# Optimization experiments

Measured on AMD Instinct MI355X. Metric: run time of the kernel, lower is better.

The kernel has to match this reference:

```python
import jax, jax.numpy as jnp
import numpy as np
from jax import lax

T, D, I, E = 4096, 1024, 1024, 32
TOP_K = 4
ROUTED_SCALING = 1.0
EPS = 1e-6


def setup_inputs() -> dict:
    key = jax.random.key(0)
    k1, k2, k3, k4, k5 = jax.random.split(key, 5)
    return {
        "hidden_states": jax.random.normal(k1, (T, D), dtype=jnp.float32),
        "gate_w": jax.random.normal(k2, (E, D), dtype=jnp.float32) * 0.02,
        "gate_up_proj": jax.random.normal(k3, (E, 2 * I, D), dtype=jnp.float32) * 0.02,
        "down_proj": jax.random.normal(k4, (E, D, I), dtype=jnp.float32) * 0.02,
        "expert_bias": jax.random.normal(k5, (E,), dtype=jnp.float32) * 0.01,
    }


def _route(hidden_states, gate_w, expert_bias):
    # router_logits: [T, E]
    logits = hidden_states @ gate_w.T
    routing_weights = jax.nn.sigmoid(logits)
    # expert bias affects selection only, not the weights
    scores = routing_weights + expert_bias[None, :]
    _, selected = lax.top_k(scores, TOP_K)                      # [T, K] int32
    w = jnp.take_along_axis(routing_weights, selected, axis=1)  # [T, K]
    w = w / (w.sum(axis=-1, keepdims=True) + EPS)               # norm_topk_prob
    w = w * ROUTED_SCALING
    return selected, w


def reference(hidden_states, gate_w, gate_up_proj, down_proj, expert_bias):
    t, d = hidden_states.shape
    selected, w = _route(hidden_states, gate_w, expert_bias)
    # dense token->expert combine weights [T, E] (top_k indices are unique per row)
    comb = jnp.zeros((t, E), dtype=hidden_states.dtype)
    comb = comb.at[jnp.arange(t)[:, None], selected].add(w)

    def body(acc, xs):
        w_gu, w_d, cw = xs                       # [2I,D], [D,I], [T]
        gu = hidden_states @ w_gu.T              # [T, 2I]
        g, u = jnp.split(gu, 2, axis=-1)
        h = jax.nn.silu(g) * u                   # [T, I]
        out = h @ w_d.T                          # [T, D]
        return acc + out * cw[:, None], None

    init = jnp.zeros_like(hidden_states)
    final, _ = lax.scan(body, init, (gate_up_proj, down_proj, comb.T))
    return final
```

## Files before the change

### kernel.cpp

```cpp
#include <hip/hip_runtime.h>
#include <hip/hip_bf16.h>
#include <cstdint>
#include <cstddef>

#define T_TOK 4096
#define DIM   1024
#define IDIM  1024
#define NEXP  32
#define TOPK  4
#define MAXT  160
#define RPAD  (MAXT*128)

typedef short sh8   __attribute__((ext_vector_type(8)));
typedef float f32x4 __attribute__((ext_vector_type(4)));

__device__ __forceinline__ short bf(float f) {
    union { float f; uint32_t u; } v; v.f = f;
    uint32_t r = (v.u + 0x7FFFu + ((v.u >> 16) & 1u)) >> 16;
    return (short)r;
}
__device__ __forceinline__ sh8 pack8(float4 a, float4 b) {
    sh8 r;
    r[0]=bf(a.x); r[1]=bf(a.y); r[2]=bf(a.z); r[3]=bf(a.w);
    r[4]=bf(b.x); r[5]=bf(b.y); r[6]=bf(b.z); r[7]=bf(b.w);
    return r;
}
__device__ __forceinline__ uint32_t cvtpk(float lo, float hi) {
    uint32_t r;
    asm("v_cvt_pk_bf16_f32 %0, %1, %2" : "=v"(r) : "v"(lo), "v"(hi));
    return r;
}
__device__ __forceinline__ sh8 cvt8(f32x4 a, f32x4 b) {
    union { uint32_t u[4]; sh8 s; } v;
    v.u[0] = cvtpk(a[0], a[1]); v.u[1] = cvtpk(a[2], a[3]);
    v.u[2] = cvtpk(b[0], b[1]); v.u[3] = cvtpk(b[2], b[3]);
    return v.s;
}
__device__ __forceinline__ void glds16(const void* g, const void* l) {
    __builtin_amdgcn_global_load_lds((const __attribute__((address_space(1))) void*)g,
                                     (__attribute__((address_space(3))) void*)l, 16, 0, 0);
}

__device__ __forceinline__ int tile_expert(const int* __restrict__ cnt, int mt, int& tile_start) {
    int s = 0, e = -1, ts = 0;
    #pragma unroll
    for (int i = 0; i < NEXP; ++i) {
        int t = (cnt[i] + 127) >> 7;
        if (mt >= s && mt < s + t) { e = i; ts = s; }
        s += t;
    }
    tile_start = ts;
    return e;
}

__device__ __forceinline__ int balanced_bid(const int* __restrict__ cnt, int ntsz) {
    int tb = 0;
    #pragma unroll
    for (int i = 0; i < NEXP; ++i) tb += (cnt[i] + 127) >> 7;
    int total = tb * ntsz;
    int q = total >> 3, r = total & 7;
    int xcd = (int)blockIdx.x & 7, pos = (int)blockIdx.x >> 3;
    int cap = q + (xcd < r ? 1 : 0);
    if (pos >= cap) return -1;
    return (xcd < r ? xcd * (q + 1) : r * (q + 1) + (xcd - r) * q) + pos;
}

__device__ __forceinline__ bool decode_wmajor(const int* __restrict__ cnt, int bid, int ntsz,
                                              int& e, int& mt, int& nt) {
    int base = 0, tacc = 0, fe = -1, floc = 0, fts = 0, fntl = 1;
    #pragma unroll
    for (int i = 0; i < NEXP; ++i) {
        int ntl = (cnt[i] + 127) >> 7;
        int sz  = ntsz * ntl;
        if (bid >= base && bid < base + sz) { fe = i; floc = bid - base; fts = tacc; fntl = ntl; }
        base += sz; tacc += ntl;
    }
    if (fe < 0) return false;
    e  = fe;
    nt = floc / fntl;
    mt = fts + (floc % fntl);
    return true;
}

__global__ __launch_bounds__(256) void router_kernel(
    const float* __restrict__ X, const float* __restrict__ GW,
    const float* __restrict__ bias, int* __restrict__ topk_idx,
    float* __restrict__ topk_w, int* __restrict__ cnt,
    int* __restrict__ tlist_c, int* __restrict__ posmap)
{
    int wid  = threadIdx.x >> 6;
    int lane = threadIdx.x & 63;
    int t = blockIdx.x * 4 + wid;

    float4 h[4];
    const float4* xr = reinterpret_cast<const float4*>(X + (size_t)t * DIM);
    #pragma unroll
    for (int c = 0; c < 4; ++c) h[c] = xr[lane + 64 * c];

    float myscore = 0.f;
    for (int e = 0; e < NEXP; ++e) {
        const float4* gr = reinterpret_cast<const float4*>(GW + (size_t)e * DIM);
        float p = 0.f;
        #pragma unroll
        for (int c = 0; c < 4; ++c) {
            float4 g = gr[lane + 64 * c];
            p += h[c].x * g.x + h[c].y * g.y + h[c].z * g.z + h[c].w * g.w;
        }
        #pragma unroll
        for (int o = 32; o; o >>= 1) p += __shfl_xor(p, o);
        if (lane == e) myscore = p;
    }
    float rw = 1.f / (1.f + expf(-myscore));
    float sel = (lane < NEXP) ? rw + bias[lane] : -1e30f;

    float wsum = 0.f;
    int   oi = 0; float ow = 0.f;
    #pragma unroll
    for (int k = 0; k < TOPK; ++k) {
        float v = sel;
        int   idx = (lane < NEXP) ? lane : 9999;
        #pragma unroll
        for (int o = 32; o; o >>= 1) {
            float v2 = __shfl_xor(v, o);
            int   i2 = __shfl_xor(idx, o);
            if (v2 > v || (v2 == v && i2 < idx)) { v = v2; idx = i2; }
        }
        float wk = __shfl(rw, idx);
        wsum += wk;
        if (lane == k)   { oi = idx; ow = wk; }
        if (lane == idx) sel = -1e30f;
    }
    if (lane < TOPK) {
        int gid = t * TOPK + lane;
        topk_idx[gid] = oi;
        topk_w  [gid] = ow / (wsum + 1e-6f);
        int pos = atomicAdd(&cnt[oi], 1);
        tlist_c[oi * T_TOK + pos] = t;
        posmap[gid] = pos;
    }
}

__global__ __launch_bounds__(256) void gather_kernel(
    const float* __restrict__ X, const int* __restrict__ cnt,
    const int* __restrict__ tlist_c, short* __restrict__ Xg)
{
    int wid = threadIdx.x >> 6, lane = threadIdx.x & 63;
    int r = blockIdx.x * 4 + wid;
    int ts;
    int e = tile_expert(cnt, r >> 7, ts);
    if (e < 0) return;
    int li = r - (ts << 7);
    bool real = li < cnt[e];
    int t = real ? tlist_c[e * T_TOK + li] : 0;
    const float4* src = reinterpret_cast<const float4*>(X + (size_t)t * DIM);
    sh8* dst = reinterpret_cast<sh8*>(Xg + (size_t)r * DIM);
    float4 z = make_float4(0.f, 0.f, 0.f, 0.f);
    #pragma unroll
    for (int it = 0; it < 2; ++it) {
        int si = it * 64 + lane;
        float4 a = real ? src[2 * si]     : z;
        float4 b = real ? src[2 * si + 1] : z;
        dst[si] = pack8(a, b);
    }
}

__global__ __launch_bounds__(256, 3) void gemm1_kernel(
    const short* __restrict__ Xg, const float* __restrict__ GUP,
    const int* __restrict__ cnt, short* __restrict__ H)
{
    int bid = balanced_bid(cnt, 16);
    if (bid < 0) return;
    int e, mt, nt;
    if (!decode_wmajor(cnt, bid, 16, e, mt, nt)) return;
    int m0 = mt * 128, n0 = nt * 64;

    __shared__ short As[128 * 64];
    __shared__ float Bg[64 * 64];
    __shared__ float Bu[64 * 64];

    int tid = threadIdx.x, lane = tid & 63, wv = tid >> 6;
    int wm = (wv >> 1) * 64, wn = (wv & 1) * 32;

    f32x4 accg[4][2] = {};
    f32x4 accu[4][2] = {};

    int swcolA = ((lane & 7) ^ (lane >> 3)) * 8;
    const float* gbase = GUP + ((size_t)e * 2 * IDIM + n0) * DIM;
    const float* ubase = gbase + (size_t)IDIM * DIM;

    auto stage = [&](int k0) {
        #pragma unroll
        for (int j = 0; j < 4; ++j) {
            int ch = wv * 4 + j;
            glds16(Xg + (size_t)(m0 + ch * 8 + (lane >> 3)) * DIM + k0 + swcolA, &As[ch * 512]);
        }
        #pragma unroll
        for (int j = 0; j < 4; ++j) {
            int ch = wv * 4 + j;
            int r  = ch * 4 + (lane >> 4);
            int sc = ((lane & 15) ^ (r & 15)) << 2;
            glds16(gbase + (size_t)r * DIM + k0 + sc, &Bg[ch * 256]);
            glds16(ubase + (size_t)r * DIM + k0 + sc, &Bu[ch * 256]);
        }
    };

    int swrA = (lane & 7) << 3;
    int rx   = lane & 15;
    for (int it = 0; it < DIM / 64; ++it) {
        stage(it * 64);
        __syncthreads();
        #pragma unroll
        for (int kk = 0; kk < 64; kk += 32) {
            int kiA = (kk + (lane >> 4) * 8) ^ swrA;
            sh8 af[4], gf[2], uf[2];
            #pragma unroll
            for (int fm = 0; fm < 4; ++fm)
                af[fm] = *reinterpret_cast<const sh8*>(&As[(wm + fm * 16 + (lane & 15)) * 64 + kiA]);
            int c0 = (kk >> 2) + (lane >> 4) * 2;
            #pragma unroll
            for (int fn = 0; fn < 2; ++fn) {
                int R = wn + fn * 16 + (lane & 15);
                const float* bg = &Bg[R * 64];
                f32x4 lo = *reinterpret_cast<const f32x4*>(&bg[(c0       ^ rx) << 2]);
                f32x4 hi = *reinterpret_cast<const f32x4*>(&bg[((c0 + 1) ^ rx) << 2]);
                gf[fn] = cvt8(lo, hi);
                const float* bu = &Bu[R * 64];
                lo = *reinterpret_cast<const f32x4*>(&bu[(c0       ^ rx) << 2]);
                hi = *reinterpret_cast<const f32x4*>(&bu[((c0 + 1) ^ rx) << 2]);
                uf[fn] = cvt8(lo, hi);
            }
            #pragma unroll
            for (int fm = 0; fm < 4; ++fm)
                #pragma unroll
                for (int fn = 0; fn < 2; ++fn) {
                    accg[fm][fn] = __builtin_amdgcn_mfma_f32_16x16x32_bf16(af[fm], gf[fn], accg[fm][fn], 0, 0, 0);
                    accu[fm][fn] = __builtin_amdgcn_mfma_f32_16x16x32_bf16(af[fm], uf[fn], accu[fm][fn], 0, 0, 0);
                }
        }
        __syncthreads();
    }

    #pragma unroll
    for (int fm = 0; fm < 4; ++fm)
        #pragma unroll
        for (int r = 0; r < 4; ++r) {
            int row = m0 + wm + fm * 16 + (lane >> 4) * 4 + r;
            #pragma unroll
            for (int fn = 0; fn < 2; ++fn) {
                int col = n0 + wn + fn * 16 + (lane & 15);
                float g = accg[fm][fn][r];
                float u = accu[fm][fn][r];
                H[(size_t)row * IDIM + col] = bf(g / (1.f + expf(-g)) * u);
            }
        }
}

__global__ __launch_bounds__(256, 3) void gemm2_kernel(
    const short* __restrict__ H, const float* __restrict__ DP,
    const int* __restrict__ cnt, float* __restrict__ Yf)
{
    int bid = balanced_bid(cnt, 8);
    if (bid < 0) return;
    int e, mt, nt;
    if (!decode_wmajor(cnt, bid, 8, e, mt, nt)) return;
    int m0 = mt * 128, n0 = nt * 128;

    __shared__ short As[128 * 64];
    __shared__ float Bs[128 * 64];

    int tid = threadIdx.x, lane = tid & 63, wv = tid >> 6;
    int wm = (wv >> 1) * 64, wn = (wv & 1) * 64;

    f32x4 acc[4][4] = {};

    int swcolA = ((lane & 7) ^ (lane >> 3)) * 8;
    const float* dbase = DP + ((size_t)e * DIM + n0) * IDIM;

    auto stage = [&](int k0) {
        #pragma unroll
        for (int j = 0; j < 4; ++j) {
            int ch = wv * 4 + j;
            glds16(H + (size_t)(m0 + ch * 8 + (lane >> 3)) * IDIM + k0 + swcolA, &As[ch * 512]);
        }
        #pragma unroll
        for (int j = 0; j < 8; ++j) {
            int ch = wv * 8 + j;
            int r  = ch * 4 + (lane >> 4);
            int sc = ((lane & 15) ^ (r & 15)) << 2;
            glds16(dbase + (size_t)r * IDIM + k0 + sc, &Bs[ch * 256]);
        }
    };

    int swrA = (lane & 7) << 3;
    int rx   = lane & 15;
    for (int it = 0; it < IDIM / 64; ++it) {
        stage(it * 64);
        __syncthreads();
        #pragma unroll
        for (int kk = 0; kk < 64; kk += 32) {
            int kiA = (kk + (lane >> 4) * 8) ^ swrA;
            sh8 af[4], bq[4];
            #pragma unroll
            for (int fm = 0; fm < 4; ++fm)
                af[fm] = *reinterpret_cast<const sh8*>(&As[(wm + fm * 16 + (lane & 15)) * 64 + kiA]);
            int c0 = (kk >> 2) + (lane >> 4) * 2;
            #pragma unroll
            for (int fn = 0; fn < 4; ++fn) {
                int R = wn + fn * 16 + (lane & 15);
                const float* bs = &Bs[R * 64];
                f32x4 lo = *reinterpret_cast<const f32x4*>(&bs[(c0       ^ rx) << 2]);
                f32x4 hi = *reinterpret_cast<const f32x4*>(&bs[((c0 + 1) ^ rx) << 2]);
                bq[fn] = cvt8(lo, hi);
            }
            #pragma unroll
            for (int fm = 0; fm < 4; ++fm)
                #pragma unroll
                for (int fn = 0; fn < 4; ++fn)
                    acc[fm][fn] = __builtin_amdgcn_mfma_f32_16x16x32_bf16(af[fm], bq[fn], acc[fm][fn], 0, 0, 0);
        }
        __syncthreads();
    }

    #pragma unroll
    for (int fm = 0; fm < 4; ++fm)
        #pragma unroll
        for (int r = 0; r < 4; ++r) {
            int row = m0 + wm + fm * 16 + (lane >> 4) * 4 + r;
            #pragma unroll
            for (int fn = 0; fn < 4; ++fn) {
                int col = n0 + wn + fn * 16 + (lane & 15);
                Yf[(size_t)row * DIM + col] = acc[fm][fn][r];
            }
        }
}

__global__ __launch_bounds__(256) void combine_kernel(
    const float* __restrict__ Yf, const int* __restrict__ cnt,
    const int* __restrict__ topk_idx, const float* __restrict__ topk_w,
    const int* __restrict__ posmap, float* __restrict__ out)
{
    int t = blockIdx.x;
    int d = threadIdx.x * 4;
    int es[TOPK], rows[TOPK];
    #pragma unroll
    for (int k = 0; k < TOPK; ++k) es[k] = topk_idx[t * TOPK + k];
    int p = 0;
    #pragma unroll
    for (int i = 0; i < NEXP; ++i) {
        #pragma unroll
        for (int k = 0; k < TOPK; ++k)
            if (es[k] == i) rows[k] = p + posmap[t * TOPK + k];
        p += ((cnt[i] + 127) >> 7) << 7;
    }
    float4 acc = make_float4(0.f, 0.f, 0.f, 0.f);
    #pragma unroll
    for (int k = 0; k < TOPK; ++k) {
        float w = topk_w[t * TOPK + k];
        float4 y = *reinterpret_cast<const float4*>(Yf + (size_t)rows[k] * DIM + d);
        acc.x += w * y.x; acc.y += w * y.y; acc.z += w * y.z; acc.w += w * y.w;
    }
    *reinterpret_cast<float4*>(out + (size_t)t * DIM + d) = acc;
}

extern "C" void kernel_launch(void* const* d_in, const int* in_sizes, int n_in,
                              void* d_out, int out_size, void* d_ws, size_t ws_size,
                              hipStream_t stream)
{
    const float* X    = (const float*)d_in[0];
    const float* GW   = (const float*)d_in[1];
    const float* GUP  = (const float*)d_in[2];
    const float* DP   = (const float*)d_in[3];
    const float* BIAS = (const float*)d_in[4];
    float* out = (float*)d_out;

    char* ws = (char*)d_ws;
    int*   cnt      = (int*)ws;
    int*   topk_idx = (int*)(ws + (4u   << 10));
    float* topk_w   = (float*)(ws + (68u  << 10));
    int*   posmap   = (int*)(ws + (132u << 10));
    int*   tlist_c  = (int*)(ws + (196u << 10));

    constexpr size_t OFF_H  = 2ull << 20;
    constexpr size_t SZ_BF  = (size_t)RPAD * IDIM * 2;
    constexpr size_t OFF_XG = OFF_H + SZ_BF;
    constexpr size_t OFF_YF = OFF_XG + SZ_BF;

    short* H  = (short*)(ws + OFF_H);
    short* Xg = (short*)(ws + OFF_XG);
    float* Yf = (float*)(ws + OFF_YF);

    (void)hipMemsetAsync(cnt, 0, 128, stream);

    router_kernel<<<T_TOK / 4, 256, 0, stream>>>(X, GW, BIAS, topk_idx, topk_w,
                                                 cnt, tlist_c, posmap);
    gather_kernel<<<RPAD / 4, 256, 0, stream>>>(X, cnt, tlist_c, Xg);

    gemm1_kernel<<<MAXT * 16, 256, 0, stream>>>(Xg, GUP, cnt, H);
    gemm2_kernel<<<MAXT * 8,  256, 0, stream>>>(H, DP, cnt, Yf);

    combine_kernel<<<T_TOK, 256, 0, stream>>>(Yf, cnt, topk_idx, topk_w, posmap, out);
}
```

Measured before the change: 329.0 us.

## Double-buffer LDS staging in both expert GEMMs with K-step of 32

Both grouped GEMM kernels now split the shared-memory tiles into two buffers of half the K depth (32 instead of 64). The next tile's global-to-LDS loads are issued before computing on the current one, and a partial vmcnt wait replaces the full synchronisation. This aims to hide global memory latency behind MFMA work. Total LDS use stays the same, but there are twice as many iterations and barriers, and correctness now depends on the hand-counted vmcnt(6) matching the number of outstanding loads.

```diff
diff --git a/kernel.cpp b/kernel.cpp
--- a/kernel.cpp
+++ b/kernel.cpp
@@ -174,9 +174,9 @@
     if (!decode_wmajor(cnt, bid, 16, e, mt, nt)) return;
     int m0 = mt * 128, n0 = nt * 64;
 
-    __shared__ short As[128 * 64];
-    __shared__ float Bg[64 * 64];
-    __shared__ float Bu[64 * 64];
+    __shared__ short As[2][128 * 32];
+    __shared__ float Bg[2][64 * 32];
+    __shared__ float Bu[2][64 * 32];
 
     int tid = threadIdx.x, lane = tid & 63, wv = tid >> 6;
     int wm = (wv >> 1) * 64, wn = (wv & 1) * 32;
@@ -184,60 +184,71 @@
     f32x4 accg[4][2] = {};
     f32x4 accu[4][2] = {};
 
-    int swcolA = ((lane & 7) ^ (lane >> 3)) * 8;
+    const short* abase = Xg + (size_t)m0 * DIM;
     const float* gbase = GUP + ((size_t)e * 2 * IDIM + n0) * DIM;
     const float* ubase = gbase + (size_t)IDIM * DIM;
 
-    auto stage = [&](int k0) {
-        #pragma unroll
-        for (int j = 0; j < 4; ++j) {
-            int ch = wv * 4 + j;
-            glds16(Xg + (size_t)(m0 + ch * 8 + (lane >> 3)) * DIM + k0 + swcolA, &As[ch * 512]);
-        }
-        #pragma unroll
-        for (int j = 0; j < 4; ++j) {
-            int ch = wv * 4 + j;
-            int r  = ch * 4 + (lane >> 4);
-            int sc = ((lane & 15) ^ (r & 15)) << 2;
-            glds16(gbase + (size_t)r * DIM + k0 + sc, &Bg[ch * 256]);
-            glds16(ubase + (size_t)r * DIM + k0 + sc, &Bu[ch * 256]);
+    int aRow = lane >> 2;
+    int aCol = ((lane & 3) ^ (aRow & 3)) * 8;
+    int bRow = lane >> 3;
+    int bCol = ((lane & 7) ^ bRow) * 4;
+
+    auto stage = [&](int b, int k0) {
+        #pragma unroll
+        for (int j = 0; j < 2; ++j) {
+            int ch = wv * 2 + j;
+            glds16(abase + (size_t)(ch * 16 + aRow) * DIM + k0 + aCol, &As[b][ch * 512]);
+        }
+        #pragma unroll
+        for (int j = 0; j < 2; ++j) {
+            int ch = wv * 2 + j;
+            glds16(gbase + (size_t)(ch * 8 + bRow) * DIM + k0 + bCol, &Bg[b][ch * 256]);
+            glds16(ubase + (size_t)(ch * 8 + bRow) * DIM + k0 + bCol, &Bu[b][ch * 256]);
         }
     };
 
-    int swrA = (lane & 7) << 3;
-    int rx   = lane & 15;
-    for (int it = 0; it < DIM / 64; ++it) {
-        stage(it * 64);
-        __syncthreads();
-        #pragma unroll
-        for (int kk = 0; kk < 64; kk += 32) {
-            int kiA = (kk + (lane >> 4) * 8) ^ swrA;
-            sh8 af[4], gf[2], uf[2];
-            #pragma unroll
-            for (int fm = 0; fm < 4; ++fm)
-                af[fm] = *reinterpret_cast<const sh8*>(&As[(wm + fm * 16 + (lane & 15)) * 64 + kiA]);
-            int c0 = (kk >> 2) + (lane >> 4) * 2;
+    int aIdx = ((lane >> 4) ^ (lane & 3)) * 8;
+    int c0b  = (lane >> 4) * 2;
+    int rxB  = lane & 7;
+
+    stage(0, 0);
+    for (int it = 0; it < DIM / 32; ++it) {
+        int c = it & 1;
+        if (it + 1 < DIM / 32) {
+            stage(c ^ 1, (it + 1) * 32);
+            asm volatile("s_waitcnt vmcnt(6)" ::: "memory");
+        } else {
+            asm volatile("s_waitcnt vmcnt(0)" ::: "memory");
+        }
+        __builtin_amdgcn_sched_barrier(0);
+        __builtin_amdgcn_s_barrier();
+
+        sh8 af[4], gf[2], uf[2];
+        #pragma unroll
+        for (int fm = 0; fm < 4; ++fm)
+            af[fm] = *reinterpret_cast<const sh8*>(&As[c][(wm + fm * 16 + (lane & 15)) * 32 + aIdx]);
+        #pragma unroll
+        for (int fn = 0; fn < 2; ++fn) {
+            int R = wn + fn * 16 + (lane & 15);
+            const float* bg = &Bg[c][R * 32];
+            f32x4 lo = *reinterpret_cast<const f32x4*>(&bg[( c0b      ^ rxB) << 2]);
+            f32x4 hi = *reinterpret_cast<const f32x4*>(&bg[((c0b + 1) ^ rxB) << 2]);
+            gf[fn] = cvt8(lo, hi);
+            const float* bu = &Bu[c][R * 32];
+            lo = *reinterpret_cast<const f32x4*>(&bu[( c0b      ^ rxB) << 2]);
+            hi = *reinterpret_cast<const f32x4*>(&bu[((c0b + 1) ^ rxB) << 2]);
+            uf[fn] = cvt8(lo, hi);
+        }
+        #pragma unroll
+        for (int fm = 0; fm < 4; ++fm)
             #pragma unroll
             for (int fn = 0; fn < 2; ++fn) {
-                int R = wn + fn * 16 + (lane & 15);
-                const float* bg = &Bg[R * 64];
-                f32x4 lo = *reinterpret_cast<const f32x4*>(&bg[(c0       ^ rx) << 2]);
-                f32x4 hi = *reinterpret_cast<const f32x4*>(&bg[((c0 + 1) ^ rx) << 2]);
-                gf[fn] = cvt8(lo, hi);
-                const float* bu = &Bu[R * 64];
-                lo = *reinterpret_cast<const f32x4*>(&bu[(c0       ^ rx) << 2]);
-                hi = *reinterpret_cast<const f32x4*>(&bu[((c0 + 1) ^ rx) << 2]);
-                uf[fn] = cvt8(lo, hi);
+                accg[fm][fn] = __builtin_amdgcn_mfma_f32_16x16x32_bf16(af[fm], gf[fn], accg[fm][fn], 0, 0, 0);
+                accu[fm][fn] = __builtin_amdgcn_mfma_f32_16x16x32_bf16(af[fm], uf[fn], accu[fm][fn], 0, 0, 0);
             }
-            #pragma unroll
-            for (int fm = 0; fm < 4; ++fm)
-                #pragma unroll
-                for (int fn = 0; fn < 2; ++fn) {
-                    accg[fm][fn] = __builtin_amdgcn_mfma_f32_16x16x32_bf16(af[fm], gf[fn], accg[fm][fn], 0, 0, 0);
-                    accu[fm][fn] = __builtin_amdgcn_mfma_f32_16x16x32_bf16(af[fm], uf[fn], accu[fm][fn], 0, 0, 0);
-                }
-        }
-        __syncthreads();
+
+        asm volatile("" ::: "memory");
+        __builtin_amdgcn_s_barrier();
     }
 
     #pragma unroll
@@ -265,60 +276,71 @@
     if (!decode_wmajor(cnt, bid, 8, e, mt, nt)) return;
     int m0 = mt * 128, n0 = nt * 128;
 
-    __shared__ short As[128 * 64];
-    __shared__ float Bs[128 * 64];
+    __shared__ short As[2][128 * 32];
+    __shared__ float Bs[2][128 * 32];
 
     int tid = threadIdx.x, lane = tid & 63, wv = tid >> 6;
     int wm = (wv >> 1) * 64, wn = (wv & 1) * 64;
 
     f32x4 acc[4][4] = {};
 
-    int swcolA = ((lane & 7) ^ (lane >> 3)) * 8;
+    const short* abase = H + (size_t)m0 * IDIM;
     const float* dbase = DP + ((size_t)e * DIM + n0) * IDIM;
 
-    auto stage = [&](int k0) {
+    int aRow = lane >> 2;
+    int aCol = ((lane & 3) ^ (aRow & 3)) * 8;
+    int bRow = lane >> 3;
+    int bCol = ((lane & 7) ^ bRow) * 4;
+
+    auto stage = [&](int b, int k0) {
+        #pragma unroll
+        for (int j = 0; j < 2; ++j) {
+            int ch = wv * 2 + j;
+            glds16(abase + (size_t)(ch * 16 + aRow) * IDIM + k0 + aCol, &As[b][ch * 512]);
+        }
         #pragma unroll
         for (int j = 0; j < 4; ++j) {
             int ch = wv * 4 + j;
-            glds16(H + (size_t)(m0 + ch * 8 + (lane >> 3)) * IDIM + k0 + swcolA, &As[ch * 512]);
-        }
-        #pragma unroll
-        for (int j = 0; j < 8; ++j) {
-            int ch = wv * 8 + j;
-            int r  = ch * 4 + (lane >> 4);
-            int sc = ((lane & 15) ^ (r & 15)) << 2;
-            glds16(dbase + (size_t)r * IDIM + k0 + sc, &Bs[ch * 256]);
+            glds16(dbase + (size_t)(ch * 8 + bRow) * IDIM + k0 + bCol, &Bs[b][ch * 256]);
         }
     };
 
-    int swrA = (lane & 7) << 3;
-    int rx   = lane & 15;
-    for (int it = 0; it < IDIM / 64; ++it) {
-        stage(it * 64);
-        __syncthreads();
-        #pragma unroll
-        for (int kk = 0; kk < 64; kk += 32) {
-            int kiA = (kk + (lane >> 4) * 8) ^ swrA;
-            sh8 af[4], bq[4];
+    int aIdx = ((lane >> 4) ^ (lane & 3)) * 8;
+    int c0b  = (lane >> 4) * 2;
+    int rxB  = lane & 7;
+
+    stage(0, 0);
+    for (int it = 0; it < IDIM / 32; ++it) {
+        int c = it & 1;
+        if (it + 1 < IDIM / 32) {
+            stage(c ^ 1, (it + 1) * 32);
+            asm volatile("s_waitcnt vmcnt(6)" ::: "memory");
+        } else {
+            asm volatile("s_waitcnt vmcnt(0)" ::: "memory");
+        }
+        __builtin_amdgcn_sched_barrier(0);
+        __builtin_amdgcn_s_barrier();
+
+        sh8 af[4], bq[4];
+        #pragma unroll
+        for (int fm = 0; fm < 4; ++fm)
+            af[fm] = *reinterpret_cast<const sh8*>(&As[c][(wm + fm * 16 + (lane & 15)) * 32 + aIdx]);
+        #pragma unroll
+        for (int fn = 0; fn < 4; ++fn) {
+            int R = wn + fn * 16 + (lane & 15);
+            const float* bs = &Bs[c][R * 32];
+            f32x4 lo = *reinterpret_cast<const f32x4*>(&bs[( c0b      ^ rxB) << 2]);
+            f32x4 hi = *reinterpret_cast<const f32x4*>(&bs[((c0b + 1) ^ rxB) << 2]);
+            bq[fn] = cvt8(lo, hi);
+        }
+        #pragma unroll
+        for (int fm = 0; fm < 4; ++fm)
             #pragma unroll
-            for (int fm = 0; fm < 4; ++fm)
-                af[fm] = *reinterpret_cast<const sh8*>(&As[(wm + fm * 16 + (lane & 15)) * 64 + kiA]);
-            int c0 = (kk >> 2) + (lane >> 4) * 2;
-            #pragma unroll
-            for (int fn = 0; fn < 4; ++fn) {
-                int R = wn + fn * 16 + (lane & 15);
-                const float* bs = &Bs[R * 64];
-                f32x4 lo = *reinterpret_cast<const f32x4*>(&bs[(c0       ^ rx) << 2]);
-                f32x4 hi = *reinterpret_cast<const f32x4*>(&bs[((c0 + 1) ^ rx) << 2]);
-                bq[fn] = cvt8(lo, hi);
-            }
-            #pragma unroll
-            for (int fm = 0; fm < 4; ++fm)
-                #pragma unroll
-                for (int fn = 0; fn < 4; ++fn)
-                    acc[fm][fn] = __builtin_amdgcn_mfma_f32_16x16x32_bf16(af[fm], bq[fn], acc[fm][fn], 0, 0, 0);
-        }
-        __syncthreads();
+            for (int fn = 0; fn < 4; ++fn)
+                acc[fm][fn] = __builtin_amdgcn_mfma_f32_16x16x32_bf16(af[fm], bq[fn], acc[fm][fn], 0, 0, 0);
+
+        asm volatile("" ::: "memory");
+        __builtin_amdgcn_s_barrier();
     }
 
     #pragma unroll
```

After: 370.3 us. 1.13x slower.

## Load fp32 expert weights straight to registers and double-buffer activation tiles

Applied to the files above, without the earlier changes.

Both expert GEMMs now read their fp32 weight fragments directly from global memory into registers, prefetched one k-step ahead, instead of staging them through LDS. The activation tile is double-buffered in LDS, so each iteration needs one barrier instead of two. gemm2 also drops to a 64-wide N tile with twice the blocks and raises its occupancy hint to 4. The intent is to cut LDS traffic and barrier stalls and to overlap loads with MFMA work. In exchange, weight loads become less coalesced (strided per-lane rows) and each block reuses the streamed weights less.

```diff
diff --git a/kernel.cpp b/kernel.cpp
--- a/kernel.cpp
+++ b/kernel.cpp
@@ -174,61 +174,65 @@
     if (!decode_wmajor(cnt, bid, 16, e, mt, nt)) return;
     int m0 = mt * 128, n0 = nt * 64;
 
-    __shared__ short As[128 * 64];
-    __shared__ float Bg[64 * 64];
-    __shared__ float Bu[64 * 64];
+    __shared__ short As[2][128 * 64];
 
     int tid = threadIdx.x, lane = tid & 63, wv = tid >> 6;
     int wm = (wv >> 1) * 64, wn = (wv & 1) * 32;
+    int l15 = lane & 15;
 
     f32x4 accg[4][2] = {};
     f32x4 accu[4][2] = {};
 
     int swcolA = ((lane & 7) ^ (lane >> 3)) * 8;
-    const float* gbase = GUP + ((size_t)e * 2 * IDIM + n0) * DIM;
-    const float* ubase = gbase + (size_t)IDIM * DIM;
-
-    auto stage = [&](int k0) {
+    int swrA   = (lane & 7) << 3;
+
+    const float* gp[2];
+    const float* up[2];
+    #pragma unroll
+    for (int fn = 0; fn < 2; ++fn) {
+        gp[fn] = GUP + ((size_t)e * 2 * IDIM + n0 + wn + fn * 16 + l15) * DIM + (lane >> 4) * 8;
+        up[fn] = gp[fn] + (size_t)IDIM * DIM;
+    }
+
+    f32x4 bg[4], bu[4];
+    auto loadB = [&](int k) {
+        #pragma unroll
+        for (int fn = 0; fn < 2; ++fn) {
+            bg[fn * 2]     = *reinterpret_cast<const f32x4*>(gp[fn] + k);
+            bg[fn * 2 + 1] = *reinterpret_cast<const f32x4*>(gp[fn] + k + 4);
+            bu[fn * 2]     = *reinterpret_cast<const f32x4*>(up[fn] + k);
+            bu[fn * 2 + 1] = *reinterpret_cast<const f32x4*>(up[fn] + k + 4);
+        }
+    };
+    auto stageA = [&](int b, int k0) {
         #pragma unroll
         for (int j = 0; j < 4; ++j) {
             int ch = wv * 4 + j;
-            glds16(Xg + (size_t)(m0 + ch * 8 + (lane >> 3)) * DIM + k0 + swcolA, &As[ch * 512]);
-        }
-        #pragma unroll
-        for (int j = 0; j < 4; ++j) {
-            int ch = wv * 4 + j;
-            int r  = ch * 4 + (lane >> 4);
-            int sc = ((lane & 15) ^ (r & 15)) << 2;
-            glds16(gbase + (size_t)r * DIM + k0 + sc, &Bg[ch * 256]);
-            glds16(ubase + (size_t)r * DIM + k0 + sc, &Bu[ch * 256]);
+            glds16(Xg + (size_t)(m0 + ch * 8 + (lane >> 3)) * DIM + k0 + swcolA, &As[b][ch * 512]);
         }
     };
 
-    int swrA = (lane & 7) << 3;
-    int rx   = lane & 15;
+    loadB(0);
+    stageA(0, 0);
     for (int it = 0; it < DIM / 64; ++it) {
-        stage(it * 64);
+        int b = it & 1;
         __syncthreads();
-        #pragma unroll
-        for (int kk = 0; kk < 64; kk += 32) {
-            int kiA = (kk + (lane >> 4) * 8) ^ swrA;
-            sh8 af[4], gf[2], uf[2];
+        if (it + 1 < DIM / 64) stageA(b ^ 1, (it + 1) * 64);
+        #pragma unroll
+        for (int kh = 0; kh < 2; ++kh) {
+            sh8 gf[2], uf[2];
+            #pragma unroll
+            for (int fn = 0; fn < 2; ++fn) {
+                gf[fn] = cvt8(bg[fn * 2], bg[fn * 2 + 1]);
+                uf[fn] = cvt8(bu[fn * 2], bu[fn * 2 + 1]);
+            }
+            int nk = it * 64 + (kh + 1) * 32;
+            if (nk < DIM) loadB(nk);
+            int kiA = (kh * 32 + (lane >> 4) * 8) ^ swrA;
+            sh8 af[4];
             #pragma unroll
             for (int fm = 0; fm < 4; ++fm)
-                af[fm] = *reinterpret_cast<const sh8*>(&As[(wm + fm * 16 + (lane & 15)) * 64 + kiA]);
-            int c0 = (kk >> 2) + (lane >> 4) * 2;
-            #pragma unroll
-            for (int fn = 0; fn < 2; ++fn) {
-                int R = wn + fn * 16 + (lane & 15);
-                const float* bg = &Bg[R * 64];
-                f32x4 lo = *reinterpret_cast<const f32x4*>(&bg[(c0       ^ rx) << 2]);
-                f32x4 hi = *reinterpret_cast<const f32x4*>(&bg[((c0 + 1) ^ rx) << 2]);
-                gf[fn] = cvt8(lo, hi);
-                const float* bu = &Bu[R * 64];
-                lo = *reinterpret_cast<const f32x4*>(&bu[(c0       ^ rx) << 2]);
-                hi = *reinterpret_cast<const f32x4*>(&bu[((c0 + 1) ^ rx) << 2]);
-                uf[fn] = cvt8(lo, hi);
-            }
+                af[fm] = *reinterpret_cast<const sh8*>(&As[b][(wm + fm * 16 + l15) * 64 + kiA]);
             #pragma unroll
             for (int fm = 0; fm < 4; ++fm)
                 #pragma unroll
@@ -237,7 +241,6 @@
                     accu[fm][fn] = __builtin_amdgcn_mfma_f32_16x16x32_bf16(af[fm], uf[fn], accu[fm][fn], 0, 0, 0);
                 }
         }
-        __syncthreads();
     }
 
     #pragma unroll
@@ -247,7 +250,7 @@
             int row = m0 + wm + fm * 16 + (lane >> 4) * 4 + r;
             #pragma unroll
             for (int fn = 0; fn < 2; ++fn) {
-                int col = n0 + wn + fn * 16 + (lane & 15);
+                int col = n0 + wn + fn * 16 + l15;
                 float g = accg[fm][fn][r];
                 float u = accu[fm][fn][r];
                 H[(size_t)row * IDIM + col] = bf(g / (1.f + expf(-g)) * u);
@@ -255,70 +258,73 @@
         }
 }
 
-__global__ __launch_bounds__(256, 3) void gemm2_kernel(
+__global__ __launch_bounds__(256, 4) void gemm2_kernel(
     const short* __restrict__ H, const float* __restrict__ DP,
     const int* __restrict__ cnt, float* __restrict__ Yf)
 {
-    int bid = balanced_bid(cnt, 8);
+    int bid = balanced_bid(cnt, 16);
     if (bid < 0) return;
     int e, mt, nt;
-    if (!decode_wmajor(cnt, bid, 8, e, mt, nt)) return;
-    int m0 = mt * 128, n0 = nt * 128;
-
-    __shared__ short As[128 * 64];
-    __shared__ float Bs[128 * 64];
+    if (!decode_wmajor(cnt, bid, 16, e, mt, nt)) return;
+    int m0 = mt * 128, n0 = nt * 64;
+
+    __shared__ short As[2][128 * 64];
 
     int tid = threadIdx.x, lane = tid & 63, wv = tid >> 6;
-    int wm = (wv >> 1) * 64, wn = (wv & 1) * 64;
-
-    f32x4 acc[4][4] = {};
+    int wm = (wv >> 1) * 64, wn = (wv & 1) * 32;
+    int l15 = lane & 15;
+
+    f32x4 acc[4][2] = {};
 
     int swcolA = ((lane & 7) ^ (lane >> 3)) * 8;
-    const float* dbase = DP + ((size_t)e * DIM + n0) * IDIM;
-
-    auto stage = [&](int k0) {
+    int swrA   = (lane & 7) << 3;
+
+    const float* dp[2];
+    #pragma unroll
+    for (int fn = 0; fn < 2; ++fn)
+        dp[fn] = DP + ((size_t)e * DIM + n0 + wn + fn * 16 + l15) * IDIM + (lane >> 4) * 8;
+
+    f32x4 bd[4];
+    auto loadB = [&](int k) {
+        #pragma unroll
+        for (int fn = 0; fn < 2; ++fn) {
+            bd[fn * 2]     = *reinterpret_cast<const f32x4*>(dp[fn] + k);
+            bd[fn * 2 + 1] = *reinterpret_cast<const f32x4*>(dp[fn] + k + 4);
+        }
+    };
+    auto stageA = [&](int b, int k0) {
         #pragma unroll
         for (int j = 0; j < 4; ++j) {
             int ch = wv * 4 + j;
-            glds16(H + (size_t)(m0 + ch * 8 + (lane >> 3)) * IDIM + k0 + swcolA, &As[ch * 512]);
-        }
-        #pragma unroll
-        for (int j = 0; j < 8; ++j) {
-            int ch = wv * 8 + j;
-            int r  = ch * 4 + (lane >> 4);
-            int sc = ((lane & 15) ^ (r & 15)) << 2;
-            glds16(dbase + (size_t)r * IDIM + k0 + sc, &Bs[ch * 256]);
+            glds16(H + (size_t)(m0 + ch * 8 + (lane >> 3)) * IDIM + k0 + swcolA, &As[b][ch * 512]);
         }
     };
 
-    int swrA = (lane & 7) << 3;
-    int rx   = lane & 15;
+    loadB(0);
+    stageA(0, 0);
     for (int it = 0; it < IDIM / 64; ++it) {
-        stage(it * 64);
+        int b = it & 1;
         __syncthreads();
-        #pragma unroll
-        for (int kk = 0; kk < 64; kk += 32) {
-            int kiA = (kk + (lane >> 4) * 8) ^ swrA;
-            sh8 af[4], bq[4];
+        if (it + 1 < IDIM / 64) stageA(b ^ 1, (it + 1) * 64);
+        #pragma unroll
+        for (int kh = 0; kh < 2; ++kh) {
+            sh8 bq[2];
+            #pragma unroll
+            for (int fn = 0; fn < 2; ++fn)
+                bq[fn] = cvt8(bd[fn * 2], bd[fn * 2 + 1]);
+            int nk = it * 64 + (kh + 1) * 32;
+            if (nk < IDIM) loadB(nk);
+            int kiA = (kh * 32 + (lane >> 4) * 8) ^ swrA;
+            sh8 af[4];
             #pragma unroll
             for (int fm = 0; fm < 4; ++fm)
-                af[fm] = *reinterpret_cast<const sh8*>(&As[(wm + fm * 16 + (lane & 15)) * 64 + kiA]);
-            int c0 = (kk >> 2) + (lane >> 4) * 2;
-            #pragma unroll
-            for (int fn = 0; fn < 4; ++fn) {
-                int R = wn + fn * 16 + (lane & 15);
-                const float* bs = &Bs[R * 64];
-                f32x4 lo = *reinterpret_cast<const f32x4*>(&bs[(c0       ^ rx) << 2]);
-                f32x4 hi = *reinterpret_cast<const f32x4*>(&bs[((c0 + 1) ^ rx) << 2]);
-                bq[fn] = cvt8(lo, hi);
-            }
+                af[fm] = *reinterpret_cast<const sh8*>(&As[b][(wm + fm * 16 + l15) * 64 + kiA]);
             #pragma unroll
             for (int fm = 0; fm < 4; ++fm)
                 #pragma unroll
-                for (int fn = 0; fn < 4; ++fn)
+                for (int fn = 0; fn < 2; ++fn)
                     acc[fm][fn] = __builtin_amdgcn_mfma_f32_16x16x32_bf16(af[fm], bq[fn], acc[fm][fn], 0, 0, 0);
         }
-        __syncthreads();
     }
 
     #pragma unroll
@@ -327,8 +333,8 @@
         for (int r = 0; r < 4; ++r) {
             int row = m0 + wm + fm * 16 + (lane >> 4) * 4 + r;
             #pragma unroll
-            for (int fn = 0; fn < 4; ++fn) {
-                int col = n0 + wn + fn * 16 + (lane & 15);
+            for (int fn = 0; fn < 2; ++fn) {
+                int col = n0 + wn + fn * 16 + l15;
                 Yf[(size_t)row * DIM + col] = acc[fm][fn][r];
             }
         }
@@ -396,7 +402,7 @@
     gather_kernel<<<RPAD / 4, 256, 0, stream>>>(X, cnt, tlist_c, Xg);
 
     gemm1_kernel<<<MAXT * 16, 256, 0, stream>>>(Xg, GUP, cnt, H);
-    gemm2_kernel<<<MAXT * 8,  256, 0, stream>>>(H, DP, cnt, Yf);
+    gemm2_kernel<<<MAXT * 16, 256, 0, stream>>>(H, DP, cnt, Yf);
 
     combine_kernel<<<T_TOK, 256, 0, stream>>>(Yf, cnt, topk_idx, topk_w, posmap, out);
 }
```

Measured after the change: 603.9 us (median of 2 runs). +83.6%, slower.

## Pre-convert down_proj to bf16 inside gemm1 grid and load bf16 in gemm2

Applied to the files above, without the earlier changes.

Appends extra blocks to the gemm1 launch that convert the fp32 down_proj weights to bf16 in a workspace buffer. gemm2 then stages bf16 B tiles with the same swizzled layout as A, which halves its shared memory for B and drops the per-iteration fp32-to-bf16 conversion. The cost is a full conversion pass over all 32 experts' down weights (128MB read, 64MB written) every call, including experts with few tokens. That pass shares the gemm1 launch and may overlap with or delay its blocks.

```diff
diff --git a/kernel.cpp b/kernel.cpp
--- a/kernel.cpp
+++ b/kernel.cpp
@@ -10,6 +10,8 @@
 #define TOPK  4
 #define MAXT  160
 #define RPAD  (MAXT*128)
+#define G1_BLOCKS (MAXT*16)
+#define CONV_BLOCKS 8192
 
 typedef short sh8   __attribute__((ext_vector_type(8)));
 typedef float f32x4 __attribute__((ext_vector_type(4)));
@@ -166,8 +168,19 @@
 
 __global__ __launch_bounds__(256, 3) void gemm1_kernel(
     const short* __restrict__ Xg, const float* __restrict__ GUP,
+    const float* __restrict__ DP, short* __restrict__ Wdb,
     const int* __restrict__ cnt, short* __restrict__ H)
 {
+    if (blockIdx.x >= G1_BLOCKS) {
+        size_t i = ((size_t)(blockIdx.x - G1_BLOCKS) * 256 + threadIdx.x) * 16;
+        f32x4 a = *reinterpret_cast<const f32x4*>(DP + i);
+        f32x4 b = *reinterpret_cast<const f32x4*>(DP + i + 4);
+        f32x4 c = *reinterpret_cast<const f32x4*>(DP + i + 8);
+        f32x4 d = *reinterpret_cast<const f32x4*>(DP + i + 12);
+        *reinterpret_cast<sh8*>(Wdb + i)     = cvt8(a, b);
+        *reinterpret_cast<sh8*>(Wdb + i + 8) = cvt8(c, d);
+        return;
+    }
     int bid = balanced_bid(cnt, 16);
     if (bid < 0) return;
     int e, mt, nt;
@@ -256,7 +269,7 @@
 }
 
 __global__ __launch_bounds__(256, 3) void gemm2_kernel(
-    const short* __restrict__ H, const float* __restrict__ DP,
+    const short* __restrict__ H, const short* __restrict__ Wdb,
     const int* __restrict__ cnt, float* __restrict__ Yf)
 {
     int bid = balanced_bid(cnt, 8);
@@ -266,15 +279,16 @@
     int m0 = mt * 128, n0 = nt * 128;
 
     __shared__ short As[128 * 64];
-    __shared__ float Bs[128 * 64];
+    __shared__ short Bs[128 * 64];
 
     int tid = threadIdx.x, lane = tid & 63, wv = tid >> 6;
     int wm = (wv >> 1) * 64, wn = (wv & 1) * 64;
+    int l15 = lane & 15;
 
     f32x4 acc[4][4] = {};
 
     int swcolA = ((lane & 7) ^ (lane >> 3)) * 8;
-    const float* dbase = DP + ((size_t)e * DIM + n0) * IDIM;
+    const short* bbase = Wdb + ((size_t)e * DIM + n0) * IDIM;
 
     auto stage = [&](int k0) {
         #pragma unroll
@@ -283,35 +297,26 @@
             glds16(H + (size_t)(m0 + ch * 8 + (lane >> 3)) * IDIM + k0 + swcolA, &As[ch * 512]);
         }
         #pragma unroll
-        for (int j = 0; j < 8; ++j) {
-            int ch = wv * 8 + j;
-            int r  = ch * 4 + (lane >> 4);
-            int sc = ((lane & 15) ^ (r & 15)) << 2;
-            glds16(dbase + (size_t)r * IDIM + k0 + sc, &Bs[ch * 256]);
+        for (int j = 0; j < 4; ++j) {
+            int ch = wv * 4 + j;
+            glds16(bbase + (size_t)(ch * 8 + (lane >> 3)) * IDIM + k0 + swcolA, &Bs[ch * 512]);
         }
     };
 
-    int swrA = (lane & 7) << 3;
-    int rx   = lane & 15;
+    int swr = (lane & 7) << 3;
     for (int it = 0; it < IDIM / 64; ++it) {
         stage(it * 64);
         __syncthreads();
         #pragma unroll
         for (int kk = 0; kk < 64; kk += 32) {
-            int kiA = (kk + (lane >> 4) * 8) ^ swrA;
+            int ki = (kk + (lane >> 4) * 8) ^ swr;
             sh8 af[4], bq[4];
             #pragma unroll
             for (int fm = 0; fm < 4; ++fm)
-                af[fm] = *reinterpret_cast<const sh8*>(&As[(wm + fm * 16 + (lane & 15)) * 64 + kiA]);
-            int c0 = (kk >> 2) + (lane >> 4) * 2;
-            #pragma unroll
-            for (int fn = 0; fn < 4; ++fn) {
-                int R = wn + fn * 16 + (lane & 15);
-                const float* bs = &Bs[R * 64];
-                f32x4 lo = *reinterpret_cast<const f32x4*>(&bs[(c0       ^ rx) << 2]);
-                f32x4 hi = *reinterpret_cast<const f32x4*>(&bs[((c0 + 1) ^ rx) << 2]);
-                bq[fn] = cvt8(lo, hi);
-            }
+                af[fm] = *reinterpret_cast<const sh8*>(&As[(wm + fm * 16 + l15) * 64 + ki]);
+            #pragma unroll
+            for (int fn = 0; fn < 4; ++fn)
+                bq[fn] = *reinterpret_cast<const sh8*>(&Bs[(wn + fn * 16 + l15) * 64 + ki]);
             #pragma unroll
             for (int fm = 0; fm < 4; ++fm)
                 #pragma unroll
@@ -328,7 +333,7 @@
             int row = m0 + wm + fm * 16 + (lane >> 4) * 4 + r;
             #pragma unroll
             for (int fn = 0; fn < 4; ++fn) {
-                int col = n0 + wn + fn * 16 + (lane & 15);
+                int col = n0 + wn + fn * 16 + l15;
                 Yf[(size_t)row * DIM + col] = acc[fm][fn][r];
             }
         }
@@ -380,14 +385,16 @@
     int*   posmap   = (int*)(ws + (132u << 10));
     int*   tlist_c  = (int*)(ws + (196u << 10));
 
-    constexpr size_t OFF_H  = 2ull << 20;
-    constexpr size_t SZ_BF  = (size_t)RPAD * IDIM * 2;
-    constexpr size_t OFF_XG = OFF_H + SZ_BF;
-    constexpr size_t OFF_YF = OFF_XG + SZ_BF;
-
-    short* H  = (short*)(ws + OFF_H);
-    short* Xg = (short*)(ws + OFF_XG);
-    float* Yf = (float*)(ws + OFF_YF);
+    constexpr size_t OFF_H   = 2ull << 20;
+    constexpr size_t SZ_BF   = (size_t)RPAD * IDIM * 2;
+    constexpr size_t OFF_XG  = OFF_H + SZ_BF;
+    constexpr size_t OFF_YF  = OFF_XG + SZ_BF;
+    constexpr size_t OFF_WDB = 192ull << 20;
+
+    short* H   = (short*)(ws + OFF_H);
+    short* Xg  = (short*)(ws + OFF_XG);
+    float* Yf  = (float*)(ws + OFF_YF);
+    short* Wdb = (short*)(ws + OFF_WDB);
 
     (void)hipMemsetAsync(cnt, 0, 128, stream);
 
@@ -395,8 +402,8 @@
                                                  cnt, tlist_c, posmap);
     gather_kernel<<<RPAD / 4, 256, 0, stream>>>(X, cnt, tlist_c, Xg);
 
-    gemm1_kernel<<<MAXT * 16, 256, 0, stream>>>(Xg, GUP, cnt, H);
-    gemm2_kernel<<<MAXT * 8,  256, 0, stream>>>(H, DP, cnt, Yf);
+    gemm1_kernel<<<G1_BLOCKS + CONV_BLOCKS, 256, 0, stream>>>(Xg, GUP, DP, Wdb, cnt, H);
+    gemm2_kernel<<<MAXT * 8, 256, 0, stream>>>(H, Wdb, cnt, Yf);
 
     combine_kernel<<<T_TOK, 256, 0, stream>>>(Yf, cnt, topk_idx, topk_w, posmap, out);
 }
```

Result: no change. 334.0 us (+1.5%).
